# Kernel optimization log

Measured on AMD Instinct MI355X. Metric: run time of the kernel, lower is better.

## Reference

```python
import jax, jax.numpy as jnp
import numpy as np

DIM = 256
HEADS = 8

def conv1x1(x, W, b):
    # x: [b,c,h,w], W: [o,c], b: [o]
    return jnp.einsum('oc,bchw->bohw', W, x) + b[None, :, None, None]

def setup_inputs() -> dict:
    key = jax.random.key(0)
    ks = jax.random.split(key, 16)
    B, C, H, Wd = 8, DIM, 96, 96
    s = 1.0 / np.sqrt(C)
    inp = {
        'x': jax.random.normal(ks[0], (B, C, H, Wd), jnp.float32),
        'y': jax.random.normal(ks[1], (B, C, H, Wd), jnp.float32),
        'z': jax.random.normal(ks[2], (B, C, H, Wd), jnp.float32),
        'W_qr': jax.random.normal(ks[3], (C // 2, C), jnp.float32) * s,
        'b_qr': jnp.zeros((C // 2,), jnp.float32),
        'W_qd': jax.random.normal(ks[4], (C // 2, C), jnp.float32) * s,
        'b_qd': jnp.zeros((C // 2,), jnp.float32),
        'W_kf': jax.random.normal(ks[5], (C, C), jnp.float32) * s,
        'b_kf': jnp.zeros((C,), jnp.float32),
        'W_vf': jax.random.normal(ks[6], (C, C), jnp.float32) * s,
        'b_vf': jnp.zeros((C,), jnp.float32),
        'W_cat': jax.random.normal(ks[7], (C, C), jnp.float32) * s,
        'b_cat': jnp.zeros((C,), jnp.float32),
        'W_proj': jax.random.normal(ks[8], (C, C), jnp.float32) * s,
        'b_proj': jnp.zeros((C,), jnp.float32),
        'temperature': jnp.ones((HEADS, 1, 1), jnp.float32),
    }
    return inp

def reference(x, y, z, W_qr, b_qr, W_qd, b_qd, W_kf, b_kf, W_vf, b_vf,
              W_cat, b_cat, W_proj, b_proj, temperature):
    b, c, h, w = x.shape
    hw = h * w
    ch = c // HEADS  # channels per head

    q_r = conv1x1(x, W_qr, b_qr)
    q_d = conv1x1(y, W_qd, b_qd)
    k_f = conv1x1(z, W_kf, b_kf)
    v_f = conv1x1(z, W_vf, b_vf)
    q = conv1x1(jnp.concatenate([q_r, q_d], axis=1), W_cat, b_cat)

    def to_heads(t):  # [b, head*ch, h, w] -> [b, head, ch, hw]
        return t.reshape(b, HEADS, ch, hw)

    q = to_heads(q)
    k = to_heads(k_f)
    v = to_heads(v_f)

    # L2-normalize along spatial axis (eps=1e-12 as in F.normalize)
    q = q / jnp.maximum(jnp.linalg.norm(q, axis=-1, keepdims=True), 1e-12)
    k = k / jnp.maximum(jnp.linalg.norm(k, axis=-1, keepdims=True), 1e-12)

    # channel attention: [b,head,ch,ch]
    attn = jnp.einsum('bhcn,bhdn->bhcd', q, k) * temperature[None]
    attn = jax.nn.softmax(attn, axis=-1)
    out = jnp.einsum('bhcd,bhdn->bhcn', attn, v)  # [b,head,ch,hw]
    out = out.reshape(b, c, h, w)
    return conv1x1(out, W_proj, b_proj) + z
```

## Files before the change

### kernel.cpp

```cpp
#include <hip/hip_runtime.h>
#include <hip/hip_bf16.h>

#define HW 9216
#define CDIM 256
#define NBATCH 8
#define NHEADS 8

typedef __bf16 bf16x8 __attribute__((ext_vector_type(8)));
typedef float f32x4 __attribute__((ext_vector_type(4)));

__device__ inline unsigned short f2bf(float f) {
    unsigned int u = __builtin_bit_cast(unsigned int, f);
    u = (u + 0x7FFF + ((u >> 16) & 1)) >> 16;
    return (unsigned short)u;
}
__device__ inline float bf2f(unsigned short s) {
    unsigned int u = ((unsigned int)s) << 16;
    return __builtin_bit_cast(float, u);
}
__device__ inline unsigned int pk2(float a, float b) {
    return (unsigned int)f2bf(a) | ((unsigned int)f2bf(b) << 16);
}
__device__ inline float ldx(const float* p) { return *p; }
__device__ inline float ldx(const unsigned short* p) { return bf2f(*p); }
__device__ inline void stx(float* p, float v) { *p = v; }
__device__ inline void stx(unsigned short* p, float v) { *p = f2bf(v); }

__global__ void fuse_wq(const float* __restrict__ W_cat, const float* __restrict__ W_qr,
                        const float* __restrict__ W_qd, const float* __restrict__ b_qr,
                        const float* __restrict__ b_qd, const float* __restrict__ b_cat,
                        unsigned short* __restrict__ Wq, float* __restrict__ bq) {
    int o = blockIdx.x;
    int c = threadIdx.x;
    float ax = 0.f, ay = 0.f;
    for (int i = 0; i < 128; ++i) {
        ax += W_cat[o * 256 + i] * W_qr[i * 256 + c];
        ay += W_cat[o * 256 + 128 + i] * W_qd[i * 256 + c];
    }
    Wq[o * 512 + c] = f2bf(ax);
    Wq[o * 512 + 256 + c] = f2bf(ay);
    if (c == 0) {
        float s = b_cat[o];
        for (int i = 0; i < 128; ++i)
            s += W_cat[o * 256 + i] * b_qr[i] + W_cat[o * 256 + 128 + i] * b_qd[i];
        bq[o] = s;
    }
}

__global__ void cvt_w(const float* __restrict__ a, const float* __restrict__ b,
                      unsigned short* __restrict__ oa, unsigned short* __restrict__ ob) {
    int i = blockIdx.x * 256 + threadIdx.x;
    oa[i] = f2bf(a[i]);
    ob[i] = f2bf(b[i]);
}

template <typename TX, typename TOut>
__global__ __launch_bounds__(256) void gemm_mfma(
    const unsigned short* __restrict__ A, int a_bs, int Ktot,
    const TX* __restrict__ X0, const TX* __restrict__ X1,
    const float* __restrict__ bias, const float* __restrict__ resid,
    TOut* __restrict__ Out) {
    const int b = blockIdx.z;
    const int n0 = blockIdx.x * 128;
    const int m0 = blockIdx.y * 128;
    const int tid = threadIdx.x;
    const int lane = tid & 63;
    const int wid = tid >> 6;
    const int wm = (wid >> 1) * 64;
    const int wn = (wid & 1) * 64;
    const int l15 = lane & 15;
    const int quad = lane >> 4;

    __shared__ __align__(16) unsigned short Bs[4 * 128 * 8];

    const unsigned short* Ab = A + (size_t)b * a_bs;
    const TX* Xb0 = X0 + (size_t)b * CDIM * HW;
    const TX* Xb1 = X1 ? X1 + (size_t)b * CDIM * HW : nullptr;

    f32x4 acc[4][4] = {};

    const int sn = tid & 127;
    const int sq0 = (tid >> 7) * 2;

    for (int k0 = 0; k0 < Ktot; k0 += 32) {
        const TX* Xp = (k0 < 256) ? Xb0 : Xb1;
        const int k0r = k0 & 255;

#pragma unroll
        for (int qq = 0; qq < 2; ++qq) {
            int q = sq0 + qq;
            const TX* src = Xp + (size_t)(k0r + q * 8) * HW + n0 + sn;
            float f[8];
#pragma unroll
            for (int j = 0; j < 8; ++j) f[j] = ldx(src + (size_t)j * HW);
            uint4 pk;
            pk.x = pk2(f[0], f[1]);
            pk.y = pk2(f[2], f[3]);
            pk.z = pk2(f[4], f[5]);
            pk.w = pk2(f[6], f[7]);
            *(uint4*)&Bs[(q * 128 + sn) * 8] = pk;
        }

        bf16x8 af[4];
#pragma unroll
        for (int mi = 0; mi < 4; ++mi)
            af[mi] = *(const bf16x8*)(Ab + (size_t)(m0 + wm + mi * 16 + l15) * Ktot + k0 + quad * 8);

        __syncthreads();

        bf16x8 bfr[4];
#pragma unroll
        for (int nj = 0; nj < 4; ++nj)
            bfr[nj] = *(const bf16x8*)&Bs[(quad * 128 + wn + nj * 16 + l15) * 8];

#pragma unroll
        for (int mi = 0; mi < 4; ++mi)
#pragma unroll
            for (int nj = 0; nj < 4; ++nj)
                acc[mi][nj] = __builtin_amdgcn_mfma_f32_16x16x32_bf16(af[mi], bfr[nj], acc[mi][nj], 0, 0, 0);

        __syncthreads();
    }

#pragma unroll
    for (int mi = 0; mi < 4; ++mi) {
#pragma unroll
        for (int r = 0; r < 4; ++r) {
            int m = m0 + wm + mi * 16 + quad * 4 + r;
            float bv = bias[m];
#pragma unroll
            for (int nj = 0; nj < 4; ++nj) {
                int n = n0 + wn + nj * 16 + l15;
                size_t off = ((size_t)b * CDIM + m) * HW + n;
                float v = acc[mi][nj][r] + bv;
                if (resid) v += resid[off];
                stx(&Out[off], v);
            }
        }
    }
}

__global__ __launch_bounds__(256) void gram_kernel(
    const unsigned short* __restrict__ q, const unsigned short* __restrict__ k,
    float* __restrict__ G, float* __restrict__ sqq, float* __restrict__ sqk) {
    const int nc = blockIdx.x;
    const int h = blockIdx.y, b = blockIdx.z;
    const int t = threadIdx.x;

    __shared__ float qs[32][128];
    __shared__ float ks[32][129];

    size_t base = ((size_t)b * CDIM + h * 32) * HW + nc * 128;
#pragma unroll
    for (int i = 0; i < 16; ++i) {
        int idx = i * 256 + t;
        int row = idx >> 7, col = idx & 127;
        qs[row][col] = bf2f(q[base + (size_t)row * HW + col]);
        ks[row][col] = bf2f(k[base + (size_t)row * HW + col]);
    }
    __syncthreads();

    const int d = t & 31;
    const int cb = t >> 5;
    float acc[4] = {0.f, 0.f, 0.f, 0.f};
    for (int n = 0; n < 128; ++n) {
        float kv = ks[d][n];
#pragma unroll
        for (int p = 0; p < 4; ++p) acc[p] += qs[cb + 8 * p][n] * kv;
    }

    float* Gp = G + (size_t)(b * 8 + h) * 32 * 32;
#pragma unroll
    for (int p = 0; p < 4; ++p) atomicAdd(&Gp[(cb + 8 * p) * 32 + d], acc[p]);

    if (t < 64) {
        int c = t & 31;
        float sq = 0.f;
        if (t < 32) {
            for (int n = 0; n < 128; ++n) { float v = qs[c][n]; sq += v * v; }
            atomicAdd(&sqq[(b * 8 + h) * 32 + c], sq);
        } else {
            for (int n = 0; n < 128; ++n) { float v = ks[c][n]; sq += v * v; }
            atomicAdd(&sqk[(b * 8 + h) * 32 + c], sq);
        }
    }
}

__global__ __launch_bounds__(1024) void softmax_kernel(
    const float* __restrict__ G, const float* __restrict__ sqq,
    const float* __restrict__ sqk, const float* __restrict__ temp,
    float* __restrict__ A) {
    int bh = blockIdx.x;
    int h = bh & 7;
    int c = threadIdx.y, d = threadIdx.x;
    float nq = fmaxf(sqrtf(sqq[bh * 32 + c]), 1e-12f);
    float nk = fmaxf(sqrtf(sqk[bh * 32 + d]), 1e-12f);
    float v = G[(size_t)(bh * 32 + c) * 32 + d] / (nq * nk) * temp[h];
    float m = v;
    for (int s = 16; s > 0; s >>= 1) m = fmaxf(m, __shfl_xor(m, s, 32));
    float e = __expf(v - m);
    float sum = e;
    for (int s = 16; s > 0; s >>= 1) sum += __shfl_xor(sum, s, 32);
    A[(size_t)(bh * 32 + c) * 32 + d] = e / sum;
}

__global__ __launch_bounds__(256) void build_m(const float* __restrict__ W_proj,
                                               const float* __restrict__ A,
                                               unsigned short* __restrict__ M) {
    int o = blockIdx.x;
    int b = blockIdx.y;
    int t = threadIdx.x;
    int h = t >> 5, d = t & 31;
    const float* Ab = A + (size_t)(b * 8 + h) * 32 * 32;
    float acc = 0.f;
    for (int c = 0; c < 32; ++c)
        acc += W_proj[o * 256 + h * 32 + c] * Ab[c * 32 + d];
    M[((size_t)b * 256 + o) * 256 + t] = f2bf(acc);
}

extern "C" void kernel_launch(void* const* d_in, const int* in_sizes, int n_in,
                              void* d_out, int out_size, void* d_ws, size_t ws_size,
                              hipStream_t stream) {
    const float* x = (const float*)d_in[0];
    const float* y = (const float*)d_in[1];
    const float* z = (const float*)d_in[2];
    const float* W_qr = (const float*)d_in[3];
    const float* b_qr = (const float*)d_in[4];
    const float* W_qd = (const float*)d_in[5];
    const float* b_qd = (const float*)d_in[6];
    const float* W_kf = (const float*)d_in[7];
    const float* b_kf = (const float*)d_in[8];
    const float* W_vf = (const float*)d_in[9];
    const float* b_vf = (const float*)d_in[10];
    const float* W_cat = (const float*)d_in[11];
    const float* b_cat = (const float*)d_in[12];
    const float* W_proj = (const float*)d_in[13];
    const float* b_proj = (const float*)d_in[14];
    const float* temp = (const float*)d_in[15];
    float* out = (float*)d_out;

    char* ws = (char*)d_ws;
    const size_t NT = (size_t)NBATCH * CDIM * HW;
    unsigned short* qb = (unsigned short*)ws;
    unsigned short* kb = qb + NT;
    unsigned short* vb = kb + NT;
    char* p = (char*)(vb + NT);
    unsigned short* Wq = (unsigned short*)p;  p += 256 * 512 * 2;
    unsigned short* Wk = (unsigned short*)p;  p += 256 * 256 * 2;
    unsigned short* Wv = (unsigned short*)p;  p += 256 * 256 * 2;
    float* bq  = (float*)p;                   p += 1024;
    float* G   = (float*)p;                   p += 64 * 32 * 32 * 4;
    float* sqq = (float*)p;                   p += 2048 * 4;
    float* sqk = (float*)p;                   p += 2048 * 4;
    float* Aat = (float*)p;                   p += 64 * 32 * 32 * 4;
    unsigned short* Mb = (unsigned short*)p;  p += (size_t)8 * 256 * 256 * 2;

    hipMemsetAsync(G, 0, 262144 + 8192 + 8192, stream);

    fuse_wq<<<256, 256, 0, stream>>>(W_cat, W_qr, W_qd, b_qr, b_qd, b_cat, Wq, bq);
    cvt_w<<<256, 256, 0, stream>>>(W_kf, W_vf, Wk, Wv);

    dim3 gg(HW / 128, CDIM / 128, NBATCH);
    gemm_mfma<float, unsigned short><<<gg, 256, 0, stream>>>(Wq, 0, 512, x, y, bq, nullptr, qb);
    gemm_mfma<float, unsigned short><<<gg, 256, 0, stream>>>(Wk, 0, 256, z, nullptr, b_kf, nullptr, kb);
    gemm_mfma<float, unsigned short><<<gg, 256, 0, stream>>>(Wv, 0, 256, z, nullptr, b_vf, nullptr, vb);

    gram_kernel<<<dim3(HW / 128, NHEADS, NBATCH), 256, 0, stream>>>(qb, kb, G, sqq, sqk);
    softmax_kernel<<<64, dim3(32, 32), 0, stream>>>(G, sqq, sqk, temp, Aat);
    build_m<<<dim3(256, 8), 256, 0, stream>>>(W_proj, Aat, Mb);

    gemm_mfma<unsigned short, float><<<gg, 256, 0, stream>>>(Mb, 256 * 256, 256, vb, nullptr, b_proj, z, out);
}
```

Baseline: 520.3 us.

## Double-buffer GEMM LDS tiles, vectorize loads, fuse K/V projections into one kernel

Replaces the GEMM kernel with a templated version that uses double-buffered, XOR-swizzled LDS tiles with a 64-wide K step, so global loads of the next tile overlap MFMA work on the current one. Activation loads are vectorized (4- or 2-wide) instead of scalar. The K and V projections of z are fused into a single dual-output kernel that reads z once and shares the B fragments. The gram kernel also gets vectorized loads. The cost is higher register pressure from the prefetch registers and dual accumulators, which could reduce occupancy.

```diff
diff --git a/kernel.cpp b/kernel.cpp
--- a/kernel.cpp
+++ b/kernel.cpp
@@ -1,5 +1,4 @@
 #include <hip/hip_runtime.h>
-#include <hip/hip_bf16.h>
 
 #define HW 9216
 #define CDIM 256
@@ -8,6 +7,10 @@
 
 typedef __bf16 bf16x8 __attribute__((ext_vector_type(8)));
 typedef float f32x4 __attribute__((ext_vector_type(4)));
+typedef float f32x2 __attribute__((ext_vector_type(2)));
+typedef unsigned short us4v __attribute__((ext_vector_type(4)));
+typedef unsigned short us2v __attribute__((ext_vector_type(2)));
+typedef unsigned int u32x4 __attribute__((ext_vector_type(4)));
 
 __device__ inline unsigned short f2bf(float f) {
     unsigned int u = __builtin_bit_cast(unsigned int, f);
@@ -21,8 +24,6 @@
 __device__ inline unsigned int pk2(float a, float b) {
     return (unsigned int)f2bf(a) | ((unsigned int)f2bf(b) << 16);
 }
-__device__ inline float ldx(const float* p) { return *p; }
-__device__ inline float ldx(const unsigned short* p) { return bf2f(*p); }
 __device__ inline void stx(float* p, float v) { *p = v; }
 __device__ inline void stx(unsigned short* p, float v) { *p = f2bf(v); }
 
@@ -54,87 +55,162 @@
     ob[i] = f2bf(b[i]);
 }
 
-template <typename TX, typename TOut>
-__global__ __launch_bounds__(256) void gemm_mfma(
-    const unsigned short* __restrict__ A, int a_bs, int Ktot,
+template <int BN, bool DUAL, typename TX, typename TOut>
+__global__ __launch_bounds__(256, 2) void gemm2(
+    const unsigned short* __restrict__ A0, const unsigned short* __restrict__ A1,
+    int a_bs, int Ktot,
     const TX* __restrict__ X0, const TX* __restrict__ X1,
-    const float* __restrict__ bias, const float* __restrict__ resid,
-    TOut* __restrict__ Out) {
+    const float* __restrict__ bias0, const float* __restrict__ bias1,
+    const float* __restrict__ resid, TOut* __restrict__ O0, TOut* __restrict__ O1) {
+    constexpr int NJ = BN / 32;
+    constexpr int NLD = (BN == 128) ? 4 : 2;
+    constexpr int BUFB = 8 * BN * 16;
+
     const int b = blockIdx.z;
-    const int n0 = blockIdx.x * 128;
+    const int n0 = blockIdx.x * BN;
     const int m0 = blockIdx.y * 128;
     const int tid = threadIdx.x;
     const int lane = tid & 63;
     const int wid = tid >> 6;
     const int wm = (wid >> 1) * 64;
-    const int wn = (wid & 1) * 64;
+    const int wn = (wid & 1) * (BN / 2);
     const int l15 = lane & 15;
     const int quad = lane >> 4;
 
-    __shared__ __align__(16) unsigned short Bs[4 * 128 * 8];
-
-    const unsigned short* Ab = A + (size_t)b * a_bs;
+    __shared__ __align__(16) char Bs[2][BUFB];
+
+    const unsigned short* Ab0 = A0 + (size_t)b * a_bs;
+    const unsigned short* Ab1 = DUAL ? A1 : nullptr;
     const TX* Xb0 = X0 + (size_t)b * CDIM * HW;
     const TX* Xb1 = X1 ? X1 + (size_t)b * CDIM * HW : nullptr;
 
-    f32x4 acc[4][4] = {};
-
-    const int sn = tid & 127;
-    const int sq0 = (tid >> 7) * 2;
-
-    for (int k0 = 0; k0 < Ktot; k0 += 32) {
-        const TX* Xp = (k0 < 256) ? Xb0 : Xb1;
-        const int k0r = k0 & 255;
-
-#pragma unroll
-        for (int qq = 0; qq < 2; ++qq) {
-            int q = sq0 + qq;
-            const TX* src = Xp + (size_t)(k0r + q * 8) * HW + n0 + sn;
-            float f[8];
-#pragma unroll
-            for (int j = 0; j < 8; ++j) f[j] = ldx(src + (size_t)j * HW);
-            uint4 pk;
-            pk.x = pk2(f[0], f[1]);
-            pk.y = pk2(f[2], f[3]);
-            pk.z = pk2(f[4], f[5]);
-            pk.w = pk2(f[6], f[7]);
-            *(uint4*)&Bs[(q * 128 + sn) * 8] = pk;
-        }
-
-        bf16x8 af[4];
-#pragma unroll
-        for (int mi = 0; mi < 4; ++mi)
-            af[mi] = *(const bf16x8*)(Ab + (size_t)(m0 + wm + mi * 16 + l15) * Ktot + k0 + quad * 8);
-
+    const int sn = (tid & 31) * NLD;
+    const int so = (tid >> 5) * 8;
+
+    f32x4 acc0[4][NJ] = {};
+    f32x4 acc1[DUAL ? 4 : 1][NJ] = {};
+    float f[8][NLD];
+
+    auto LOADS = [&](int kg) {
+        const TX* Xp = (Xb1 && kg >= 256) ? Xb1 : Xb0;
+        const int kr = kg & 255;
+#pragma unroll
+        for (int r = 0; r < 8; ++r) {
+            const TX* p = Xp + (size_t)(kr + so + r) * HW + n0 + sn;
+            if constexpr (sizeof(TX) == 4) {
+                if constexpr (NLD == 4) {
+                    f32x4 v = *(const f32x4*)p;
+#pragma unroll
+                    for (int j = 0; j < 4; ++j) f[r][j] = v[j];
+                } else {
+                    f32x2 v = *(const f32x2*)p;
+                    f[r][0] = v[0]; f[r][1] = v[1];
+                }
+            } else {
+                if constexpr (NLD == 4) {
+                    us4v v = *(const us4v*)p;
+#pragma unroll
+                    for (int j = 0; j < 4; ++j) f[r][j] = bf2f(v[j]);
+                } else {
+                    us2v v = *(const us2v*)p;
+                    f[r][0] = bf2f(v[0]); f[r][1] = bf2f(v[1]);
+                }
+            }
+        }
+    };
+
+    auto PKW = [&](int buf) {
+        char* base = &Bs[buf][0];
+#pragma unroll
+        for (int j = 0; j < NLD; ++j) {
+            int n = sn + j;
+            u32x4 w;
+            w[0] = pk2(f[0][j], f[1][j]);
+            w[1] = pk2(f[2][j], f[3][j]);
+            w[2] = pk2(f[4][j], f[5][j]);
+            w[3] = pk2(f[6][j], f[7][j]);
+            *(u32x4*)(base + ((((so >> 3) * BN + n) * 16) ^ ((n & 0x38) << 1))) = w;
+        }
+    };
+
+    auto COMPUTE = [&](int buf, int k0) {
+        const char* base = &Bs[buf][0];
+#pragma unroll
+        for (int kk = 0; kk < 64; kk += 32) {
+            bf16x8 bfr[NJ];
+#pragma unroll
+            for (int nj = 0; nj < NJ; ++nj) {
+                int n = wn + nj * 16 + l15;
+                bfr[nj] = *(const bf16x8*)(base +
+                    (((((kk >> 3) + quad) * BN + n) * 16) ^ ((n & 0x38) << 1)));
+            }
+            bf16x8 af[4];
+#pragma unroll
+            for (int mi = 0; mi < 4; ++mi)
+                af[mi] = *(const bf16x8*)(Ab0 + (size_t)(m0 + wm + mi * 16 + l15) * Ktot +
+                                          k0 + kk + quad * 8);
+#pragma unroll
+            for (int mi = 0; mi < 4; ++mi)
+#pragma unroll
+                for (int nj = 0; nj < NJ; ++nj)
+                    acc0[mi][nj] = __builtin_amdgcn_mfma_f32_16x16x32_bf16(af[mi], bfr[nj],
+                                                                           acc0[mi][nj], 0, 0, 0);
+            if constexpr (DUAL) {
+#pragma unroll
+                for (int mi = 0; mi < 4; ++mi)
+                    af[mi] = *(const bf16x8*)(Ab1 + (size_t)(m0 + wm + mi * 16 + l15) * Ktot +
+                                              k0 + kk + quad * 8);
+#pragma unroll
+                for (int mi = 0; mi < 4; ++mi)
+#pragma unroll
+                    for (int nj = 0; nj < NJ; ++nj)
+                        acc1[mi][nj] = __builtin_amdgcn_mfma_f32_16x16x32_bf16(af[mi], bfr[nj],
+                                                                               acc1[mi][nj], 0, 0, 0);
+            }
+        }
+    };
+
+    const int nt = Ktot >> 6;
+    LOADS(0);
+    PKW(0);
+    for (int t = 0; t < nt - 1; ++t) {
+        LOADS((t + 1) << 6);
         __syncthreads();
-
-        bf16x8 bfr[4];
-#pragma unroll
-        for (int nj = 0; nj < 4; ++nj)
-            bfr[nj] = *(const bf16x8*)&Bs[(quad * 128 + wn + nj * 16 + l15) * 8];
-
-#pragma unroll
-        for (int mi = 0; mi < 4; ++mi)
-#pragma unroll
-            for (int nj = 0; nj < 4; ++nj)
-                acc[mi][nj] = __builtin_amdgcn_mfma_f32_16x16x32_bf16(af[mi], bfr[nj], acc[mi][nj], 0, 0, 0);
-
-        __syncthreads();
-    }
+        COMPUTE(t & 1, t << 6);
+        PKW((t + 1) & 1);
+    }
+    __syncthreads();
+    COMPUTE((nt - 1) & 1, (nt - 1) << 6);
 
 #pragma unroll
     for (int mi = 0; mi < 4; ++mi) {
 #pragma unroll
         for (int r = 0; r < 4; ++r) {
             int m = m0 + wm + mi * 16 + quad * 4 + r;
-            float bv = bias[m];
-#pragma unroll
-            for (int nj = 0; nj < 4; ++nj) {
+            float bv = bias0[m];
+#pragma unroll
+            for (int nj = 0; nj < NJ; ++nj) {
                 int n = n0 + wn + nj * 16 + l15;
                 size_t off = ((size_t)b * CDIM + m) * HW + n;
-                float v = acc[mi][nj][r] + bv;
+                float v = acc0[mi][nj][r] + bv;
                 if (resid) v += resid[off];
-                stx(&Out[off], v);
+                stx(&O0[off], v);
+            }
+        }
+    }
+    if constexpr (DUAL) {
+#pragma unroll
+        for (int mi = 0; mi < 4; ++mi) {
+#pragma unroll
+            for (int r = 0; r < 4; ++r) {
+                int m = m0 + wm + mi * 16 + quad * 4 + r;
+                float bv = bias1[m];
+#pragma unroll
+                for (int nj = 0; nj < NJ; ++nj) {
+                    int n = n0 + wn + nj * 16 + l15;
+                    size_t off = ((size_t)b * CDIM + m) * HW + n;
+                    stx(&O1[off], acc1[mi][nj][r] + bv);
+                }
             }
         }
     }
@@ -152,11 +228,16 @@
 
     size_t base = ((size_t)b * CDIM + h * 32) * HW + nc * 128;
 #pragma unroll
-    for (int i = 0; i < 16; ++i) {
+    for (int i = 0; i < 4; ++i) {
         int idx = i * 256 + t;
-        int row = idx >> 7, col = idx & 127;
-        qs[row][col] = bf2f(q[base + (size_t)row * HW + col]);
-        ks[row][col] = bf2f(k[base + (size_t)row * HW + col]);
+        int row = idx >> 5, c4 = (idx & 31) * 4;
+        us4v qv = *(const us4v*)(q + base + (size_t)row * HW + c4);
+        us4v kv = *(const us4v*)(k + base + (size_t)row * HW + c4);
+#pragma unroll
+        for (int j = 0; j < 4; ++j) {
+            qs[row][c4 + j] = bf2f(qv[j]);
+            ks[row][c4 + j] = bf2f(kv[j]);
+        }
     }
     __syncthreads();
 
@@ -260,14 +341,15 @@
     fuse_wq<<<256, 256, 0, stream>>>(W_cat, W_qr, W_qd, b_qr, b_qd, b_cat, Wq, bq);
     cvt_w<<<256, 256, 0, stream>>>(W_kf, W_vf, Wk, Wv);
 
-    dim3 gg(HW / 128, CDIM / 128, NBATCH);
-    gemm_mfma<float, unsigned short><<<gg, 256, 0, stream>>>(Wq, 0, 512, x, y, bq, nullptr, qb);
-    gemm_mfma<float, unsigned short><<<gg, 256, 0, stream>>>(Wk, 0, 256, z, nullptr, b_kf, nullptr, kb);
-    gemm_mfma<float, unsigned short><<<gg, 256, 0, stream>>>(Wv, 0, 256, z, nullptr, b_vf, nullptr, vb);
+    gemm2<128, false, float, unsigned short><<<dim3(HW / 128, 2, NBATCH), 256, 0, stream>>>(
+        Wq, nullptr, 0, 512, x, y, bq, nullptr, nullptr, qb, nullptr);
+    gemm2<64, true, float, unsigned short><<<dim3(HW / 64, 2, NBATCH), 256, 0, stream>>>(
+        Wk, Wv, 0, 256, z, nullptr, b_kf, b_vf, nullptr, kb, vb);
 
     gram_kernel<<<dim3(HW / 128, NHEADS, NBATCH), 256, 0, stream>>>(qb, kb, G, sqq, sqk);
     softmax_kernel<<<64, dim3(32, 32), 0, stream>>>(G, sqq, sqk, temp, Aat);
     build_m<<<dim3(256, 8), 256, 0, stream>>>(W_proj, Aat, Mb);
 
-    gemm_mfma<unsigned short, float><<<gg, 256, 0, stream>>>(Mb, 256 * 256, 256, vb, nullptr, b_proj, z, out);
-}
+    gemm2<128, false, unsigned short, float><<<dim3(HW / 128, 2, NBATCH), 256, 0, stream>>>(
+        Mb, nullptr, 256 * 256, 256, vb, nullptr, b_proj, nullptr, z, out, nullptr);
+}
```

Result: slower. 567.4 us (+9.0%).
